# Kernel tuning notes

Hardware: AMD Instinct MI355X
Metric: run time of the kernel (lower is better)

The kernel has to match this reference:

```python
import jax, jax.numpy as jnp
import numpy as np
import math

NHID = 8; NHEADS = 8; ALPHA = 0.2; EMB = 64  # nhid*nheads must equal selfattention embed_dim=64
NPROT = 2048; NDRUG = 1500; FPROT = 512; FDRUG = 256; NPAIR = 16384


def _layernorm(x, g, b):
    m = x.mean(-1, keepdims=True)
    v = ((x - m) ** 2).mean(-1, keepdims=True)
    return (x - m) / jnp.sqrt(v + 1e-5) * g + b


def _gat(h, adj, W, a):
    # W: [H,F,O], a: [H,2O].  e_ij = leakyrelu(Wh_i . a1 + Wh_j . a2)
    # (equivalent to the repeat_interleave/repeat/cat construction in the torch code)
    Wh = jnp.einsum('nf,hfo->hno', h, W)                 # [H,N,O]
    s1 = jnp.einsum('hno,ho->hn', Wh, a[:, :NHID])       # [H,N]
    s2 = jnp.einsum('hno,ho->hn', Wh, a[:, NHID:])       # [H,N]
    e = s1[:, :, None] + s2[:, None, :]                  # [H,N,N]
    e = jnp.where(e > 0, e, ALPHA * e)                   # LeakyReLU(alpha)
    e = jnp.where(adj[None, :, :] > 0, e, jnp.float32(-9e15))
    attn = jax.nn.softmax(e, axis=-1)
    out = jax.nn.relu(jnp.einsum('hnm,hmo->hno', attn, Wh))
    H, N, O = out.shape
    return out.transpose(1, 0, 2).reshape(N, H * O)      # concat heads along dim 1


def _mhsa_sum(x, W, b):
    # Sum of NHEADS independent selfattention(64, NHEADS) modules applied to x[None].
    # x: [N,EMB]; W: [3,M,EMB,EMB] torch (out,in) layout; b: [3,M,EMB]
    M = W.shape[1]; N = x.shape[0]; hd = EMB // NHEADS
    qkv = jnp.einsum('nd,smod->smno', x, W) + b[:, :, None, :]   # [3,M,N,EMB]
    q, k, v = [t.reshape(M, N, NHEADS, hd) for t in (qkv[0], qkv[1], qkv[2])]
    scores = jnp.einsum('mnhd,mkhd->mhnk', q, k) / math.sqrt(hd)
    attn = jax.nn.softmax(scores, axis=-1)
    out = jnp.einsum('mhnk,mkhd->mnhd', attn, v).reshape(M, N, EMB)
    return out.sum(0)


def _branch(h, adj, g1W, g1a, p1W, s1W, s1b, l1g, l1b, g2W, g2a, p2W, s2W, s2b, l2g, l2b):
    x = _gat(h, adj, g1W, g1a) @ p1W.T
    x = _layernorm(_mhsa_sum(x, s1W, s1b) + x, l1g, l1b)
    x = _gat(x, adj, g2W, g2a) @ p2W.T
    x = _layernorm(_mhsa_sum(x, s2W, s2b) + x, l2g, l2b)
    return x


def _forward(fl, idx):
    (pf, padj, df, dadj,
     pg1W, pg1a, pp1W, ps1W, ps1b, pl1g, pl1b, pg2W, pg2a, pp2W, ps2W, ps2b, pl2g, pl2b,
     dg1W, dg1a, dp1W, ds1W, ds1b, dl1g, dl1b, dg2W, dg2a, dp2W, ds2W, ds2b, dl2g, dl2b,
     fc1W, fc1b, fc2W, fc2b, fc3W, fc3b) = fl
    px = _branch(pf, padj, pg1W, pg1a, pp1W, ps1W, ps1b, pl1g, pl1b, pg2W, pg2a, pp2W, ps2W, ps2b, pl2g, pl2b)
    dx = _branch(df, dadj, dg1W, dg1a, dp1W, ds1W, ds1b, dl1g, dl1b, dg2W, dg2a, dp2W, ds2W, ds2b, dl2g, dl2b)
    x = jnp.concatenate([px[idx[:, 0]], dx[idx[:, 1]]], axis=1)   # [B, 2*EMB]
    x = jax.nn.relu(x @ fc1W.T + fc1b)
    x = jax.nn.relu(x @ fc2W.T + fc2b)
    return (x @ fc3W.T + fc3b)[:, 0]


def setup_inputs() -> dict:
    key = jax.random.key(0)
    ks = iter(jax.random.split(key, 80))
    nk = lambda: next(ks)
    rn = lambda shape, s=0.1: jax.random.normal(nk(), shape, jnp.float32) * s

    def adj(n):
        a = (jax.random.uniform(nk(), (n, n)) < 0.05).astype(jnp.float32)
        return jnp.maximum(a, jnp.eye(n, dtype=jnp.float32))

    inp = {}
    inp['protein_features'] = rn((NPROT, FPROT), 1.0)
    inp['protein_adj'] = adj(NPROT)
    inp['drug_features'] = rn((NDRUG, FDRUG), 1.0)
    inp['drug_adj'] = adj(NDRUG)
    ip = jax.random.randint(nk(), (NPAIR,), 0, NPROT)
    idd = jax.random.randint(nk(), (NPAIR,), 0, NDRUG)
    inp['idx_protein_drug'] = jnp.stack([ip, idd], axis=1).astype(jnp.int32)
    for pref, F in (('p', FPROT), ('d', FDRUG)):
        inp[pref + '_gat1_W'] = rn((NHEADS, F, NHID))
        inp[pref + '_gat1_a'] = rn((NHEADS, 2 * NHID))
        inp[pref + '_pro1_W'] = rn((EMB, EMB))
        inp[pref + '_sa1_W'] = rn((3, NHEADS, EMB, EMB))
        inp[pref + '_sa1_b'] = jnp.zeros((3, NHEADS, EMB), jnp.float32)
        inp[pref + '_ln1_g'] = jnp.ones((EMB,), jnp.float32)
        inp[pref + '_ln1_b'] = jnp.zeros((EMB,), jnp.float32)
        inp[pref + '_gat2_W'] = rn((NHEADS, EMB, NHID))
        inp[pref + '_gat2_a'] = rn((NHEADS, 2 * NHID))
        inp[pref + '_pro2_W'] = rn((EMB, EMB))
        inp[pref + '_sa2_W'] = rn((3, NHEADS, EMB, EMB))
        inp[pref + '_sa2_b'] = jnp.zeros((3, NHEADS, EMB), jnp.float32)
        inp[pref + '_ln2_g'] = jnp.ones((EMB,), jnp.float32)
        inp[pref + '_ln2_b'] = jnp.zeros((EMB,), jnp.float32)
    inp['fc1_W'] = rn((2 * EMB, 2 * EMB)); inp['fc1_b'] = jnp.zeros((2 * EMB,), jnp.float32)
    inp['fc2_W'] = rn((2 * EMB, 2 * EMB)); inp['fc2_b'] = jnp.zeros((2 * EMB,), jnp.float32)
    inp['fc3_W'] = rn((1, 2 * EMB)); inp['fc3_b'] = jnp.zeros((1,), jnp.float32)
    return inp


def reference(protein_features, protein_adj, drug_features, drug_adj, idx_protein_drug,
              p_gat1_W, p_gat1_a, p_pro1_W, p_sa1_W, p_sa1_b, p_ln1_g, p_ln1_b,
              p_gat2_W, p_gat2_a, p_pro2_W, p_sa2_W, p_sa2_b, p_ln2_g, p_ln2_b,
              d_gat1_W, d_gat1_a, d_pro1_W, d_sa1_W, d_sa1_b, d_ln1_g, d_ln1_b,
              d_gat2_W, d_gat2_a, d_pro2_W, d_sa2_W, d_sa2_b, d_ln2_g, d_ln2_b,
              fc1_W, fc1_b, fc2_W, fc2_b, fc3_W, fc3_b):
    fl = (protein_features, protein_adj, drug_features, drug_adj,
          p_gat1_W, p_gat1_a, p_pro1_W, p_sa1_W, p_sa1_b, p_ln1_g, p_ln1_b,
          p_gat2_W, p_gat2_a, p_pro2_W, p_sa2_W, p_sa2_b, p_ln2_g, p_ln2_b,
          d_gat1_W, d_gat1_a, d_pro1_W, d_sa1_W, d_sa1_b, d_ln1_g, d_ln1_b,
          d_gat2_W, d_gat2_a, d_pro2_W, d_sa2_W, d_sa2_b, d_ln2_g, d_ln2_b,
          fc1_W, fc1_b, fc2_W, fc2_b, fc3_W, fc3_b)
    return _forward(fl, idx_protein_drug)
```

## Files before the change

### kernel.cpp

```cpp
#include <hip/hip_runtime.h>
#include <math.h>

#define NHID 8
#define NHEADS 8
#define EMB 64
#define NPROT 2048
#define NDRUG 1500
#define NPAIR 16384

typedef _Float16 h2 __attribute__((ext_vector_type(2)));
typedef float f4 __attribute__((ext_vector_type(4)));

__global__ void k_gat_wh(const float* __restrict__ h, const float* __restrict__ W,
                         float* __restrict__ Wh, int N, int F) {
    int idx = blockIdx.x * 256 + threadIdx.x;
    int total = NHEADS * N * NHID;
    if (idx >= total) return;
    int o  = idx & 7;
    int n  = (idx >> 3) % N;
    int hh = idx / (N * 8);
    const float4* hp4 = (const float4*)(h + (size_t)n * F);
    const float* wp = W + (size_t)hh * F * 8 + o;
    float acc = 0.f;
    for (int f4i = 0; f4i < (F >> 2); ++f4i) {
        float4 hv = hp4[f4i];
        int fb = f4i * 32;
        acc = fmaf(hv.x, wp[fb], fmaf(hv.y, wp[fb + 8],
              fmaf(hv.z, wp[fb + 16], fmaf(hv.w, wp[fb + 24], acc))));
    }
    Wh[idx] = acc;
}

__global__ void k_gat_s(const float* __restrict__ Wh, const float* __restrict__ a,
                        float* __restrict__ s1, float* __restrict__ s2, int N) {
    int idx = blockIdx.x * 256 + threadIdx.x;
    if (idx >= NHEADS * N) return;
    int hh = idx / N;
    const float* wp = Wh + (size_t)idx * 8;
    const float* ap = a + hh * 16;
    float x1 = 0.f, x2 = 0.f;
    for (int o = 0; o < 8; ++o) { x1 += wp[o] * ap[o]; x2 += wp[o] * ap[8 + o]; }
    s1[idx] = x1; s2[idx] = x2;
}

__global__ void k_gat_attn(const float* __restrict__ adj, const float* __restrict__ s1,
                           const float* __restrict__ s2, const float* __restrict__ Wh,
                           float* __restrict__ out, int N) {
    __shared__ int nbr[2048];
    __shared__ int s_cnt;
    int i = blockIdx.x;
    int tid = threadIdx.x;
    if (tid == 0) s_cnt = 0;
    __syncthreads();
    const float* arow = adj + (size_t)i * N;
    for (int j = tid; j < N; j += 256)
        if (arow[j] > 0.f) { int p = atomicAdd(&s_cnt, 1); nbr[p] = j; }
    __syncthreads();
    int cnt = s_cnt;
    int g  = tid >> 5;
    int ln = tid & 31;
    float si = s1[g * N + i];
    const float* s2h = s2 + g * N;
    float mx = -1e30f;
    for (int t = ln; t < cnt; t += 32) {
        float e = si + s2h[nbr[t]];
        e = e > 0.f ? e : 0.2f * e;
        mx = fmaxf(mx, e);
    }
    #pragma unroll
    for (int off = 16; off; off >>= 1) mx = fmaxf(mx, __shfl_xor(mx, off, 32));
    float acc[8] = {0, 0, 0, 0, 0, 0, 0, 0};
    float lsum = 0.f;
    for (int t = ln; t < cnt; t += 32) {
        int j = nbr[t];
        float e = si + s2h[j];
        e = e > 0.f ? e : 0.2f * e;
        float p = __expf(e - mx);
        lsum += p;
        const float4* wp = (const float4*)(Wh + ((size_t)g * N + j) * 8);
        float4 w0 = wp[0], w1 = wp[1];
        acc[0] += p * w0.x; acc[1] += p * w0.y; acc[2] += p * w0.z; acc[3] += p * w0.w;
        acc[4] += p * w1.x; acc[5] += p * w1.y; acc[6] += p * w1.z; acc[7] += p * w1.w;
    }
    #pragma unroll
    for (int off = 16; off; off >>= 1) {
        lsum += __shfl_xor(lsum, off, 32);
        #pragma unroll
        for (int d = 0; d < 8; ++d) acc[d] += __shfl_xor(acc[d], off, 32);
    }
    if (ln == 0) {
        float inv = 1.f / lsum;
        #pragma unroll
        for (int d = 0; d < 8; ++d) {
            float r = acc[d] * inv;
            out[(size_t)i * 64 + g * 8 + d] = r > 0.f ? r : 0.f;
        }
    }
}

__global__ void k_proj(const float* __restrict__ in, const float* __restrict__ W,
                       float* __restrict__ out, int N) {
    int idx = blockIdx.x * 256 + threadIdx.x;
    if (idx >= N * 64) return;
    int o = idx & 63, n = idx >> 6;
    const float* ip = in + (size_t)n * 64;
    const float* wp = W + (size_t)o * 64;
    float acc = 0.f;
    for (int d = 0; d < 64; ++d) acc += ip[d] * wp[d];
    out[idx] = acc;
}

__global__ void k_qkv(const float* __restrict__ x, const float* __restrict__ W,
                      const float* __restrict__ b, float* __restrict__ qkv, int N) {
    int idx = blockIdx.x * 256 + threadIdx.x;
    int total = 24 * N * 64;
    if (idx >= total) return;
    int o = idx & 63;
    int n = (idx >> 6) % N;
    int sm = idx / (N * 64);
    const float4* xp4 = (const float4*)(x + (size_t)n * 64);
    const float4* wp4 = (const float4*)(W + ((size_t)sm * 64 + o) * 64);
    float acc = b[sm * 64 + o];
    #pragma unroll 4
    for (int d4 = 0; d4 < 16; ++d4) {
        float4 xv = xp4[d4], wv = wp4[d4];
        acc = fmaf(xv.x, wv.x, fmaf(xv.y, wv.y, fmaf(xv.z, wv.z, fmaf(xv.w, wv.w, acc))));
    }
    qkv[(size_t)sm * N * 64 + (size_t)(o >> 3) * N * 8 + (size_t)n * 8 + (o & 7)] = acc;
}

#define QLOADH(qa, qb, qc, qd, r) { int row_ = row0 + (r); if (row_ >= N) row_ = 0; \
    const f4* qp_ = (const f4*)(qsl + (size_t)row_ * 8);                          \
    f4 a_ = qp_[0], b_ = qp_[1];                                                  \
    qa = h2{(_Float16)(a_.x * qs), (_Float16)(a_.y * qs)};                        \
    qb = h2{(_Float16)(a_.z * qs), (_Float16)(a_.w * qs)};                        \
    qc = h2{(_Float16)(b_.x * qs), (_Float16)(b_.y * qs)};                        \
    qd = h2{(_Float16)(b_.z * qs), (_Float16)(b_.w * qs)}; }

#define ROWSTEPH(qa, qb, qc, qd, ca, cb, lr) {                                    \
    float s_ = __builtin_amdgcn_fdot2(qa, kk0,                                    \
               __builtin_amdgcn_fdot2(qb, kk1,                                    \
               __builtin_amdgcn_fdot2(qc, kk2,                                    \
               __builtin_amdgcn_fdot2(qd, kk3, 0.f, false), false), false), false);\
    float p_ = __builtin_amdgcn_exp2f(s_); lr += p_;                              \
    f4 pv_ = {p_, p_, p_, p_};                                                    \
    ca = __builtin_elementwise_fma(pv_, vv0, ca);                                 \
    cb = __builtin_elementwise_fma(pv_, vv1, cb); }

#define BF3A(v) { v += __shfl_xor(v, 1, 64); v += __shfl_xor(v, 2, 64);           \
                  v += __shfl_xor(v, 4, 64); }

#define ROWOUT(ca, cb, lr, r) {                                                   \
    float ax_ = ca.x, ay_ = ca.y, az_ = ca.z, aw_ = ca.w;                         \
    float bx_ = cb.x, by_ = cb.y, bz_ = cb.z, bw_ = cb.w;                         \
    BF3A(ax_); BF3A(ay_); BF3A(az_); BF3A(aw_);                                   \
    BF3A(bx_); BF3A(by_); BF3A(bz_); BF3A(bw_); BF3A(lr);                         \
    int sel_ = ln & 7;                                                            \
    float t_ = (sel_ == 0) ? ax_ : (sel_ == 1) ? ay_ : (sel_ == 2) ? az_ :        \
               (sel_ == 3) ? aw_ : (sel_ == 4) ? bx_ : (sel_ == 5) ? by_ :        \
               (sel_ == 6) ? bz_ : bw_;                                           \
    t_ += __shfl_xor(t_, 8, 64); t_ += __shfl_xor(t_, 16, 64);                    \
    t_ += __shfl_xor(t_, 32, 64);                                                 \
    lr += __shfl_xor(lr, 8, 64); lr += __shfl_xor(lr, 16, 64);                    \
    lr += __shfl_xor(lr, 32, 64);                                                 \
    int row_ = row0 + (r);                                                        \
    if (ln < 8 && row_ < N)                                                       \
        atomicAdd(&accum[(size_t)row_ * 64 + hh * 8 + ln], t_ / (lr - phantom)); }

__global__ __launch_bounds__(256, 3)
void k_attn(const float* __restrict__ qkv, float* __restrict__ accum, int N) {
    __shared__ f4 kvt[256];
    int bid = blockIdx.x;
    int m  = bid & 7;
    int hh = (bid >> 3) & 7;
    int rt = bid >> 6;
    int wid = threadIdx.x >> 6, ln = threadIdx.x & 63;
    int row0 = rt * 32 + wid * 8;
    const float* qsl = qkv + (size_t)m        * N * 64 + (size_t)hh * N * 8;
    const float* ksl = qkv + (size_t)(8 + m)  * N * 64 + (size_t)hh * N * 8;
    const float* vsl = qkv + (size_t)(16 + m) * N * 64 + (size_t)hh * N * 8;

    const float qs = 0.35355339059327373f * 1.44269504088896341f;
    h2 q0a, q0b, q0c, q0d, q1a, q1b, q1c, q1d, q2a, q2b, q2c, q2d, q3a, q3b, q3c, q3d;
    h2 q4a, q4b, q4c, q4d, q5a, q5b, q5c, q5d, q6a, q6b, q6c, q6d, q7a, q7b, q7c, q7d;
    QLOADH(q0a, q0b, q0c, q0d, 0) QLOADH(q1a, q1b, q1c, q1d, 1)
    QLOADH(q2a, q2b, q2c, q2d, 2) QLOADH(q3a, q3b, q3c, q3d, 3)
    QLOADH(q4a, q4b, q4c, q4d, 4) QLOADH(q5a, q5b, q5c, q5d, 5)
    QLOADH(q6a, q6b, q6c, q6d, 6) QLOADH(q7a, q7b, q7c, q7d, 7)

    int sj = threadIdx.x >> 2;
    int part = threadIdx.x & 3;
    bool isK = (part == 0) | (part == 3);
    const float* sb = isK ? ksl : vsl;
    int halfo = (part & 2) ? 4 : 0;
    int slot_base = isK ? 0 : (part == 1 ? 1 : 2);
    int slot = slot_base ^ ((sj >> 1) & 3);
    f4* vdst = &kvt[sj * 4 + slot];
    float2* kdst = (float2*)((char*)&kvt[sj * 4 + slot] + ((part == 3) ? 8 : 0));

    f4 zf4 = {0.f, 0.f, 0.f, 0.f};
    int Tt = (N + 63) >> 6;
    f4 pre = (sj < N) ? *(const f4*)(sb + (size_t)sj * 8 + halfo) : zf4;

    float l0 = 0.f, l1 = 0.f, l2 = 0.f, l3 = 0.f, l4 = 0.f, l5 = 0.f, l6 = 0.f, l7 = 0.f;
    f4 c0a = zf4, c0b = zf4, c1a = zf4, c1b = zf4, c2a = zf4, c2b = zf4, c3a = zf4, c3b = zf4;
    f4 c4a = zf4, c4b = zf4, c5a = zf4, c5b = zf4, c6a = zf4, c6b = zf4, c7a = zf4, c7b = zf4;

    int sw = (ln >> 1) & 3;
    const f4* rbase = &kvt[ln * 4];

    for (int t = 0; t < Tt; ++t) {
        __syncthreads();
        if (isK) {
            h2 lo = h2{(_Float16)pre.x, (_Float16)pre.y};
            h2 hi = h2{(_Float16)pre.z, (_Float16)pre.w};
            float2 st;
            st.x = __builtin_bit_cast(float, lo);
            st.y = __builtin_bit_cast(float, hi);
            *kdst = st;
        } else {
            *vdst = pre;
        }
        __syncthreads();
        if (t + 1 < Tt) {
            int j = (t + 1) * 64 + sj;
            pre = (j < N) ? *(const f4*)(sb + (size_t)j * 8 + halfo) : zf4;
        }
        f4 kf = rbase[0 ^ sw];
        h2 kk0 = __builtin_bit_cast(h2, kf.x);
        h2 kk1 = __builtin_bit_cast(h2, kf.y);
        h2 kk2 = __builtin_bit_cast(h2, kf.z);
        h2 kk3 = __builtin_bit_cast(h2, kf.w);
        f4 vv0 = rbase[1 ^ sw], vv1 = rbase[2 ^ sw];
        ROWSTEPH(q0a, q0b, q0c, q0d, c0a, c0b, l0)
        ROWSTEPH(q1a, q1b, q1c, q1d, c1a, c1b, l1)
        ROWSTEPH(q2a, q2b, q2c, q2d, c2a, c2b, l2)
        ROWSTEPH(q3a, q3b, q3c, q3d, c3a, c3b, l3)
        ROWSTEPH(q4a, q4b, q4c, q4d, c4a, c4b, l4)
        ROWSTEPH(q5a, q5b, q5c, q5d, c5a, c5b, l5)
        ROWSTEPH(q6a, q6b, q6c, q6d, c6a, c6b, l6)
        ROWSTEPH(q7a, q7b, q7c, q7d, c7a, c7b, l7)
    }

    float phantom = (float)(Tt * 64 - N);
    ROWOUT(c0a, c0b, l0, 0) ROWOUT(c1a, c1b, l1, 1)
    ROWOUT(c2a, c2b, l2, 2) ROWOUT(c3a, c3b, l3, 3)
    ROWOUT(c4a, c4b, l4, 4) ROWOUT(c5a, c5b, l5, 5)
    ROWOUT(c6a, c6b, l6, 6) ROWOUT(c7a, c7b, l7, 7)
}

__global__ void k_ln(const float* __restrict__ acc, const float* __restrict__ resid,
                     const float* __restrict__ g, const float* __restrict__ b,
                     float* __restrict__ out, int N) {
    int r = blockIdx.x * 4 + (threadIdx.x >> 6);
    int d = threadIdx.x & 63;
    if (r >= N) return;
    float v = acc[(size_t)r * 64 + d] + resid[(size_t)r * 64 + d];
    float s = v;
    for (int off = 32; off; off >>= 1) s += __shfl_xor(s, off, 64);
    float mean = s * (1.f / 64.f);
    float c = v - mean;
    float vv = c * c;
    for (int off = 32; off; off >>= 1) vv += __shfl_xor(vv, off, 64);
    float var = vv * (1.f / 64.f);
    out[(size_t)r * 64 + d] = c * rsqrtf(var + 1e-5f) * g[d] + b[d];
}

#define MLP_STEP(ai, xi) {                                                        \
    ai.x = fmaf(xi.x, w0.x, fmaf(xi.y, w0.y, fmaf(xi.z, w0.z, fmaf(xi.w, w0.w, ai.x)))); \
    ai.y = fmaf(xi.x, w1.x, fmaf(xi.y, w1.y, fmaf(xi.z, w1.z, fmaf(xi.w, w1.w, ai.y)))); \
    ai.z = fmaf(xi.x, w2.x, fmaf(xi.y, w2.y, fmaf(xi.z, w2.z, fmaf(xi.w, w2.w, ai.z)))); \
    ai.w = fmaf(xi.x, w3.x, fmaf(xi.y, w3.y, fmaf(xi.z, w3.z, fmaf(xi.w, w3.w, ai.w)))); }

#define MLP_LAYER(B_)                                                             \
    a0 = z4; a1 = z4; a2 = z4; a3 = z4; a4 = z4; a5 = z4; a6 = z4; a7 = z4;       \
    _Pragma("unroll 4")                                                           \
    for (int k4 = 0; k4 < 32; ++k4) {                                             \
        float4 w0 = sW4[og][k4 ^ swz];                                            \
        float4 w1 = sW4[og + 32][k4 ^ swz];                                       \
        float4 w2 = sW4[og + 64][k4 ^ swz];                                       \
        float4 w3 = sW4[og + 96][k4 ^ swz];                                       \
        float4 x0 = sX4[pb + 0][k4], x1 = sX4[pb + 1][k4];                        \
        float4 x2 = sX4[pb + 2][k4], x3 = sX4[pb + 3][k4];                        \
        float4 x4 = sX4[pb + 4][k4], x5 = sX4[pb + 5][k4];                        \
        float4 x6 = sX4[pb + 6][k4], x7 = sX4[pb + 7][k4];                        \
        MLP_STEP(a0, x0) MLP_STEP(a1, x1) MLP_STEP(a2, x2) MLP_STEP(a3, x3)       \
        MLP_STEP(a4, x4) MLP_STEP(a5, x5) MLP_STEP(a6, x6) MLP_STEP(a7, x7)       \
    }                                                                             \
    {                                                                             \
        float bo0 = B_[og], bo1 = B_[og + 32], bo2 = B_[og + 64], bo3 = B_[og + 96]; \
        a0.x += bo0; a0.y += bo1; a0.z += bo2; a0.w += bo3;                       \
        a1.x += bo0; a1.y += bo1; a1.z += bo2; a1.w += bo3;                       \
        a2.x += bo0; a2.y += bo1; a2.z += bo2; a2.w += bo3;                       \
        a3.x += bo0; a3.y += bo1; a3.z += bo2; a3.w += bo3;                       \
        a4.x += bo0; a4.y += bo1; a4.z += bo2; a4.w += bo3;                       \
        a5.x += bo0; a5.y += bo1; a5.z += bo2; a5.w += bo3;                       \
        a6.x += bo0; a6.y += bo1; a6.z += bo2; a6.w += bo3;                       \
        a7.x += bo0; a7.y += bo1; a7.z += bo2; a7.w += bo3;                       \
    }

#define MLP_HWRITE(ai, i) {                                                       \
    float* hp_ = sXf + (size_t)(pb + (i)) * 128;                                  \
    hp_[og]      = ai.x > 0.f ? ai.x : 0.f;                                       \
    hp_[og + 32] = ai.y > 0.f ? ai.y : 0.f;                                       \
    hp_[og + 64] = ai.z > 0.f ? ai.z : 0.f;                                       \
    hp_[og + 96] = ai.w > 0.f ? ai.w : 0.f; }

#define MLP_WLOAD(Wg_) {                                                          \
    const float4* wsrc_ = (const float4*)(Wg_);                                   \
    _Pragma("unroll")                                                             \
    for (int u = 0; u < 16; ++u) {                                                \
        int f4i = u * 256 + t;                                                    \
        int o_ = f4i >> 5, k4_ = f4i & 31;                                        \
        sW4[o_][k4_ ^ (o_ & 7)] = wsrc_[f4i];                                     \
    } }

__global__ __launch_bounds__(256, 1)
void k_mlp(const float* __restrict__ px, const float* __restrict__ dx,
           const int* __restrict__ pairs,
           const float* __restrict__ W1, const float* __restrict__ b1,
           const float* __restrict__ W2, const float* __restrict__ b2,
           const float* __restrict__ W3, const float* __restrict__ b3,
           float* __restrict__ out) {
    __shared__ float4 sX4[64][32];
    __shared__ float4 sW4[128][32];
    float* sXf = (float*)sX4;
    int t = threadIdx.x;
    int base = blockIdx.x * 64;

    #pragma unroll
    for (int u = 0; u < 8; ++u) {
        int idx = u * 256 + t;
        int p = idx >> 5, c4 = idx & 31;
        int ip = pairs[(base + p) * 2], id = pairs[(base + p) * 2 + 1];
        float4 v = (c4 < 16) ? ((const float4*)px)[(size_t)ip * 16 + c4]
                             : ((const float4*)dx)[(size_t)id * 16 + (c4 - 16)];
        sX4[p][c4] = v;
    }
    MLP_WLOAD(W1)
    __syncthreads();

    int og = t & 31;
    int pb = (t >> 5) * 8;
    int swz = og & 7;
    float4 z4 = make_float4(0.f, 0.f, 0.f, 0.f);
    float4 a0, a1, a2, a3, a4, a5, a6, a7;

    MLP_LAYER(b1)
    __syncthreads();
    MLP_HWRITE(a0, 0) MLP_HWRITE(a1, 1) MLP_HWRITE(a2, 2) MLP_HWRITE(a3, 3)
    MLP_HWRITE(a4, 4) MLP_HWRITE(a5, 5) MLP_HWRITE(a6, 6) MLP_HWRITE(a7, 7)
    MLP_WLOAD(W2)
    __syncthreads();

    MLP_LAYER(b2)
    __syncthreads();
    MLP_HWRITE(a0, 0) MLP_HWRITE(a1, 1) MLP_HWRITE(a2, 2) MLP_HWRITE(a3, 3)
    MLP_HWRITE(a4, 4) MLP_HWRITE(a5, 5) MLP_HWRITE(a6, 6) MLP_HWRITE(a7, 7)
    __syncthreads();

    {
        int p = t >> 2, qd = t & 3;
        const float4* w3 = (const float4*)W3;
        float sum = 0.f;
        #pragma unroll
        for (int u = 0; u < 8; ++u) {
            float4 h = sX4[p][qd * 8 + u];
            float4 w = w3[qd * 8 + u];
            sum += h.x * w.x + h.y * w.y + h.z * w.z + h.w * w.w;
        }
        sum += __shfl_xor(sum, 1, 64);
        sum += __shfl_xor(sum, 2, 64);
        if ((t & 3) == 0) out[base + p] = sum + b3[0];
    }
}

extern "C" void kernel_launch(void* const* d_in, const int* in_sizes, int n_in,
                              void* d_out, int out_size, void* d_ws, size_t ws_size,
                              hipStream_t stream) {
    const float* pfeat = (const float*)d_in[0];
    const float* padj  = (const float*)d_in[1];
    const float* dfeat = (const float*)d_in[2];
    const float* dadj  = (const float*)d_in[3];
    const int*   pairs = (const int*)d_in[4];
    const float* fc1W = (const float*)d_in[33];
    const float* fc1b = (const float*)d_in[34];
    const float* fc2W = (const float*)d_in[35];
    const float* fc2b = (const float*)d_in[36];
    const float* fc3W = (const float*)d_in[37];
    const float* fc3b = (const float*)d_in[38];

    float* ws = (float*)d_ws;
    float* buf_Wh   = ws;
    float* buf_s1   = buf_Wh   + 8 * 2048 * 8;
    float* buf_s2   = buf_s1   + 8 * 2048;
    float* buf_gat  = buf_s2   + 8 * 2048;
    float* buf_proj = buf_gat  + 2048 * 64;
    float* buf_qkv  = buf_proj + 2048 * 64;
    float* buf_acc  = buf_qkv  + 24 * 2048 * 64;
    float* buf_x    = buf_acc  + 2048 * 64;
    float* buf_px   = buf_x    + 2048 * 64;
    float* buf_dx   = buf_px   + 2048 * 64;

    auto run_branch = [&](const float* feat, const float* adj, int N, int F,
                          void* const* w, float* xout) {
        const float* g1W = (const float*)w[0];
        const float* g1a = (const float*)w[1];
        const float* p1W = (const float*)w[2];
        const float* s1W = (const float*)w[3];
        const float* s1b = (const float*)w[4];
        const float* l1g = (const float*)w[5];
        const float* l1b = (const float*)w[6];
        const float* g2W = (const float*)w[7];
        const float* g2a = (const float*)w[8];
        const float* p2W = (const float*)w[9];
        const float* s2W = (const float*)w[10];
        const float* s2b = (const float*)w[11];
        const float* l2g = (const float*)w[12];
        const float* l2b = (const float*)w[13];

        int attnGrid = 64 * ((N + 31) / 32);

        k_gat_wh<<<(64 * N + 255) / 256, 256, 0, stream>>>(feat, g1W, buf_Wh, N, F);
        k_gat_s<<<(8 * N + 255) / 256, 256, 0, stream>>>(buf_Wh, g1a, buf_s1, buf_s2, N);
        k_gat_attn<<<N, 256, 0, stream>>>(adj, buf_s1, buf_s2, buf_Wh, buf_gat, N);
        k_proj<<<(64 * N + 255) / 256, 256, 0, stream>>>(buf_gat, p1W, buf_proj, N);
        k_qkv<<<(1536 * N + 255) / 256, 256, 0, stream>>>(buf_proj, s1W, s1b, buf_qkv, N);
        hipMemsetAsync(buf_acc, 0, (size_t)N * 64 * sizeof(float), stream);
        k_attn<<<attnGrid, 256, 0, stream>>>(buf_qkv, buf_acc, N);
        k_ln<<<(N + 3) / 4, 256, 0, stream>>>(buf_acc, buf_proj, l1g, l1b, buf_x, N);
        k_gat_wh<<<(64 * N + 255) / 256, 256, 0, stream>>>(buf_x, g2W, buf_Wh, N, EMB);
        k_gat_s<<<(8 * N + 255) / 256, 256, 0, stream>>>(buf_Wh, g2a, buf_s1, buf_s2, N);
        k_gat_attn<<<N, 256, 0, stream>>>(adj, buf_s1, buf_s2, buf_Wh, buf_gat, N);
        k_proj<<<(64 * N + 255) / 256, 256, 0, stream>>>(buf_gat, p2W, buf_proj, N);
        k_qkv<<<(1536 * N + 255) / 256, 256, 0, stream>>>(buf_proj, s2W, s2b, buf_qkv, N);
        hipMemsetAsync(buf_acc, 0, (size_t)N * 64 * sizeof(float), stream);
        k_attn<<<attnGrid, 256, 0, stream>>>(buf_qkv, buf_acc, N);
        k_ln<<<(N + 3) / 4, 256, 0, stream>>>(buf_acc, buf_proj, l2g, l2b, xout, N);
    };

    run_branch(pfeat, padj, NPROT, 512, d_in + 5, buf_px);
    run_branch(dfeat, dadj, NDRUG, 256, d_in + 19, buf_dx);

    k_mlp<<<NPAIR / 64, 256, 0, stream>>>(buf_px, buf_dx, pairs,
                                          fc1W, fc1b, fc2W, fc2b, fc3W, fc3b,
                                          (float*)d_out);
}
```

Baseline: 1.199 ms.

## Load K/V directly from global memory in attention, dropping LDS staging

The attention kernel no longer stages K/V tiles through shared memory with two barriers per tile. Each lane now reads its own key/value row straight from global memory, converting K to fp16 in registers, and a masked tail handles the remainder. Launch bounds are relaxed from 3 to 1 blocks per SU. This removes the barrier and LDS traffic, but all four waves now load the same K/V rows redundantly through cache. The looser launch bound may also let register use grow and lower occupancy.

```diff
diff --git a/kernel.cpp b/kernel.cpp
--- a/kernel.cpp
+++ b/kernel.cpp
@@ -147,6 +147,20 @@
     ca = __builtin_elementwise_fma(pv_, vv0, ca);                                 \
     cb = __builtin_elementwise_fma(pv_, vv1, cb); }
 
+#define TILEBODY {                                                                \
+    h2 kk0 = h2{(_Float16)ka.x, (_Float16)ka.y};                                  \
+    h2 kk1 = h2{(_Float16)ka.z, (_Float16)ka.w};                                  \
+    h2 kk2 = h2{(_Float16)kb.x, (_Float16)kb.y};                                  \
+    h2 kk3 = h2{(_Float16)kb.z, (_Float16)kb.w};                                  \
+    ROWSTEPH(q0a, q0b, q0c, q0d, c0a, c0b, l0)                                    \
+    ROWSTEPH(q1a, q1b, q1c, q1d, c1a, c1b, l1)                                    \
+    ROWSTEPH(q2a, q2b, q2c, q2d, c2a, c2b, l2)                                    \
+    ROWSTEPH(q3a, q3b, q3c, q3d, c3a, c3b, l3)                                    \
+    ROWSTEPH(q4a, q4b, q4c, q4d, c4a, c4b, l4)                                    \
+    ROWSTEPH(q5a, q5b, q5c, q5d, c5a, c5b, l5)                                    \
+    ROWSTEPH(q6a, q6b, q6c, q6d, c6a, c6b, l6)                                    \
+    ROWSTEPH(q7a, q7b, q7c, q7d, c7a, c7b, l7) }
+
 #define BF3A(v) { v += __shfl_xor(v, 1, 64); v += __shfl_xor(v, 2, 64);           \
                   v += __shfl_xor(v, 4, 64); }
 
@@ -167,9 +181,8 @@
     if (ln < 8 && row_ < N)                                                       \
         atomicAdd(&accum[(size_t)row_ * 64 + hh * 8 + ln], t_ / (lr - phantom)); }
 
-__global__ __launch_bounds__(256, 3)
+__global__ __launch_bounds__(256, 1)
 void k_attn(const float* __restrict__ qkv, float* __restrict__ accum, int N) {
-    __shared__ f4 kvt[256];
     int bid = blockIdx.x;
     int m  = bid & 7;
     int hh = (bid >> 3) & 7;
@@ -188,61 +201,34 @@
     QLOADH(q4a, q4b, q4c, q4d, 4) QLOADH(q5a, q5b, q5c, q5d, 5)
     QLOADH(q6a, q6b, q6c, q6d, 6) QLOADH(q7a, q7b, q7c, q7d, 7)
 
-    int sj = threadIdx.x >> 2;
-    int part = threadIdx.x & 3;
-    bool isK = (part == 0) | (part == 3);
-    const float* sb = isK ? ksl : vsl;
-    int halfo = (part & 2) ? 4 : 0;
-    int slot_base = isK ? 0 : (part == 1 ? 1 : 2);
-    int slot = slot_base ^ ((sj >> 1) & 3);
-    f4* vdst = &kvt[sj * 4 + slot];
-    float2* kdst = (float2*)((char*)&kvt[sj * 4 + slot] + ((part == 3) ? 8 : 0));
-
+    const float* kp = ksl + (size_t)ln * 8;
+    const float* vp = vsl + (size_t)ln * 8;
+
+    float l0 = 0.f, l1 = 0.f, l2 = 0.f, l3 = 0.f, l4 = 0.f, l5 = 0.f, l6 = 0.f, l7 = 0.f;
     f4 zf4 = {0.f, 0.f, 0.f, 0.f};
-    int Tt = (N + 63) >> 6;
-    f4 pre = (sj < N) ? *(const f4*)(sb + (size_t)sj * 8 + halfo) : zf4;
-
-    float l0 = 0.f, l1 = 0.f, l2 = 0.f, l3 = 0.f, l4 = 0.f, l5 = 0.f, l6 = 0.f, l7 = 0.f;
     f4 c0a = zf4, c0b = zf4, c1a = zf4, c1b = zf4, c2a = zf4, c2b = zf4, c3a = zf4, c3b = zf4;
     f4 c4a = zf4, c4b = zf4, c5a = zf4, c5b = zf4, c6a = zf4, c6b = zf4, c7a = zf4, c7b = zf4;
 
-    int sw = (ln >> 1) & 3;
-    const f4* rbase = &kvt[ln * 4];
-
-    for (int t = 0; t < Tt; ++t) {
-        __syncthreads();
-        if (isK) {
-            h2 lo = h2{(_Float16)pre.x, (_Float16)pre.y};
-            h2 hi = h2{(_Float16)pre.z, (_Float16)pre.w};
-            float2 st;
-            st.x = __builtin_bit_cast(float, lo);
-            st.y = __builtin_bit_cast(float, hi);
-            *kdst = st;
-        } else {
-            *vdst = pre;
-        }
-        __syncthreads();
-        if (t + 1 < Tt) {
-            int j = (t + 1) * 64 + sj;
-            pre = (j < N) ? *(const f4*)(sb + (size_t)j * 8 + halfo) : zf4;
-        }
-        f4 kf = rbase[0 ^ sw];
-        h2 kk0 = __builtin_bit_cast(h2, kf.x);
-        h2 kk1 = __builtin_bit_cast(h2, kf.y);
-        h2 kk2 = __builtin_bit_cast(h2, kf.z);
-        h2 kk3 = __builtin_bit_cast(h2, kf.w);
-        f4 vv0 = rbase[1 ^ sw], vv1 = rbase[2 ^ sw];
-        ROWSTEPH(q0a, q0b, q0c, q0d, c0a, c0b, l0)
-        ROWSTEPH(q1a, q1b, q1c, q1d, c1a, c1b, l1)
-        ROWSTEPH(q2a, q2b, q2c, q2d, c2a, c2b, l2)
-        ROWSTEPH(q3a, q3b, q3c, q3d, c3a, c3b, l3)
-        ROWSTEPH(q4a, q4b, q4c, q4d, c4a, c4b, l4)
-        ROWSTEPH(q5a, q5b, q5c, q5d, c5a, c5b, l5)
-        ROWSTEPH(q6a, q6b, q6c, q6d, c6a, c6b, l6)
-        ROWSTEPH(q7a, q7b, q7c, q7d, c7a, c7b, l7)
-    }
-
-    float phantom = (float)(Tt * 64 - N);
+    int Tfull = N >> 6;
+    int rem = N & 63;
+    for (int t = 0; t < Tfull; ++t) {
+        f4 ka = *(const f4*)kp;
+        f4 kb = *(const f4*)(kp + 4);
+        f4 vv0 = *(const f4*)vp;
+        f4 vv1 = *(const f4*)(vp + 4);
+        kp += 512; vp += 512;
+        TILEBODY
+    }
+    if (rem) {
+        bool ok = ln < rem;
+        f4 ka = ok ? *(const f4*)kp : zf4;
+        f4 kb = ok ? *(const f4*)(kp + 4) : zf4;
+        f4 vv0 = ok ? *(const f4*)vp : zf4;
+        f4 vv1 = ok ? *(const f4*)(vp + 4) : zf4;
+        TILEBODY
+    }
+
+    float phantom = rem ? (float)(64 - rem) : 0.f;
     ROWOUT(c0a, c0b, l0, 0) ROWOUT(c1a, c1b, l1, 1)
     ROWOUT(c2a, c2b, l2, 2) ROWOUT(c3a, c3b, l3, 3)
     ROWOUT(c4a, c4b, l4, 4) ROWOUT(c5a, c5b, l5, 5)
```

New measurement: 1.155 ms. 1.04x faster.
